# Optimization experiments

Measured on AMD Instinct MI355X. Metric: run time of the kernel, lower is better.

Reference implementation:

```python
import jax, jax.numpy as jnp
import numpy as np

S, IN, OUT = 2048, 512, 512
H, KV = 16, 4            # query heads, kv heads (cross-broadcast + averaged)
DQ = DK = DV = 64        # per-head embedding dims


def setup_inputs() -> dict:
    key = jax.random.key(0)
    ks = jax.random.split(key, 5)
    lim_in = 1.0 / np.sqrt(IN)
    lim_o = 1.0 / np.sqrt(H * DV)
    x = jax.random.normal(ks[0], (S, IN), dtype=jnp.float32)
    Wq = jax.random.uniform(ks[1], (H * DQ, IN), jnp.float32, -lim_in, lim_in)
    Wk = jax.random.uniform(ks[2], (KV * DK, IN), jnp.float32, -lim_in, lim_in)
    Wv = jax.random.uniform(ks[3], (KV * DV, IN), jnp.float32, -lim_in, lim_in)
    Wo = jax.random.uniform(ks[4], (OUT, H * DV), jnp.float32, -lim_o, lim_o)
    return {"x": x, "Wq": Wq, "Wk": Wk, "Wv": Wv, "Wo": Wo}


def reference(x, Wq, Wk, Wv, Wo):
    seq = x.shape[0]
    # projections (eqx.nn.Linear: y = W @ x, no bias)
    q = (x @ Wq.T).reshape(seq, H, DQ)    # [S, H, DQ]
    k = (x @ Wk.T).reshape(seq, KV, DK)   # [S, KV, DK]
    v = (x @ Wv.T).reshape(seq, KV, DV)   # [S, KV, DV]
    # cross-broadcast every kv head against every query head -> [KV, H, S, S]
    scores = jnp.einsum('shd,tkd->khst', q, k) / jnp.sqrt(jnp.asarray(DK, x.dtype))
    # NOTE: original applies causal mask whenever `mask is not None`; the
    # boolean flag is always passed, so masking is effectively always on.
    causal = jnp.tril(jnp.ones((seq, seq), dtype=bool))
    scores = jnp.where(causal, scores, -jnp.inf)
    w = jax.nn.softmax(scores, axis=-1)   # [KV, H, S, S]
    # attn @ V, then sum over kv heads and average by KV
    o = jnp.einsum('khst,tkd->shd', w, v) / KV  # [S, H, DV]
    return o.reshape(seq, H * DV) @ Wo.T        # [S, OUT]
```

## Files before the change

### kernel.cpp

```cpp
#include <hip/hip_runtime.h>
#include <hip/hip_bf16.h>

#define SEQ   2048
#define INF_  512
#define HQ    16
#define KVH   4
#define DH    64
#define NQ    (HQ*DH)
#define NKV   (KVH*DH)
#define OUTD  512

typedef short v8s __attribute__((ext_vector_type(8)));
typedef float v4f __attribute__((ext_vector_type(4)));

static __device__ __forceinline__ float bf2f(unsigned short u) {
    union { unsigned int i; float f; } c;
    c.i = ((unsigned int)u) << 16;
    return c.f;
}
static __device__ __forceinline__ unsigned short f2bf(float f) {
    union { float f; unsigned int i; } c; c.f = f;
    unsigned int lsb = (c.i >> 16) & 1u;
    c.i += 0x7fffu + lsb;
    return (unsigned short)(c.i >> 16);
}
static __device__ __forceinline__ unsigned int f2bf2(float lo, float hi) {
    union { __hip_bfloat162 h; unsigned int u; } c;
    c.h = __float22bfloat162_rn(make_float2(lo, hi));
    return c.u;
}
static __device__ __forceinline__ v8s pack8(v4f a, v4f b) {
    union { v8s s; uint4 u; } c;
    c.u = make_uint4(f2bf2(a[0], a[1]), f2bf2(a[2], a[3]),
                     f2bf2(b[0], b[1]), f2bf2(b[2], b[3]));
    return c.s;
}

static __device__ __forceinline__ void gll16(const void* g, void* l) {
    __builtin_amdgcn_global_load_lds(
        (const __attribute__((address_space(1))) void*)g,
        (__attribute__((address_space(3))) void*)l, 16, 0, 0);
}

static __device__ __forceinline__ void stage_tile(
    const unsigned short* __restrict__ src, int stride, int kb,
    unsigned short* ldsbase, int w, int lane)
{
#pragma unroll
    for (int i = 0; i < 2; i++) {
        const int rl = w * 16 + i * 8 + (lane >> 3);
        const int kc = ((lane & 7) ^ (rl & 7)) * 8;
        gll16(src + (size_t)rl * stride + kb + kc,
              ldsbase + (w * 16 + i * 8) * 64);
    }
}

#define QSCALE 0.180336880f

__global__ __launch_bounds__(256) void cast_all(
    const float* __restrict__ x,  const float* __restrict__ Wq,
    const float* __restrict__ Wk, const float* __restrict__ Wv,
    const float* __restrict__ Wo,
    unsigned short* __restrict__ xb,  unsigned short* __restrict__ Wqb,
    unsigned short* __restrict__ Wkb, unsigned short* __restrict__ Wvb,
    unsigned short* __restrict__ Wob)
{
    size_t i = ((size_t)blockIdx.x * 256 + threadIdx.x) * 8;
    const float* s; unsigned short* d; size_t off;
    if (i < 1048576)      { s = x;  d = xb;  off = i; }
    else if (i < 1572864) { s = Wq; d = Wqb; off = i - 1048576; }
    else if (i < 1703936) { s = Wk; d = Wkb; off = i - 1572864; }
    else if (i < 1835008) { s = Wv; d = Wvb; off = i - 1703936; }
    else                  { s = Wo; d = Wob; off = i - 1835008; }
    float4 a = *(const float4*)(s + off);
    float4 b = *(const float4*)(s + off + 4);
    *(uint4*)(d + off) = make_uint4(f2bf2(a.x, a.y), f2bf2(a.z, a.w),
                                    f2bf2(b.x, b.y), f2bf2(b.z, b.w));
}

__global__ __launch_bounds__(256, 4) void gemm_qkv(
    const unsigned short* __restrict__ xb,
    const unsigned short* __restrict__ Wqb,
    const unsigned short* __restrict__ Wkb,
    const unsigned short* __restrict__ Wvb,
    unsigned short* __restrict__ Qg,
    unsigned short* __restrict__ Kg,
    unsigned short* __restrict__ Vg)
{
    __shared__ unsigned short Asb[2][4096];
    __shared__ unsigned short Bsb[2][4096];

    const int m0 = blockIdx.x * 64;
    const int n0 = blockIdx.y * 64;

    const unsigned short* Bp; int role;
    if (n0 < NQ)            { Bp = Wqb + (size_t)n0 * INF_;              role = 0; }
    else if (n0 < NQ + NKV) { Bp = Wkb + (size_t)(n0 - NQ) * INF_;       role = 1; }
    else                    { Bp = Wvb + (size_t)(n0 - NQ - NKV) * INF_; role = 2; }

    const int tid = threadIdx.x;
    const int w = tid >> 6, lane = tid & 63;
    const int n = lane & 15, quad = lane >> 4;
    const int m7 = n & 7;
    const int r0w = (w & 1) * 32, c0w = (w >> 1) * 32;
    const unsigned short* Ap = xb + (size_t)m0 * INF_;

    v4f acc[2][2];
#pragma unroll
    for (int rt = 0; rt < 2; rt++)
#pragma unroll
        for (int ct = 0; ct < 2; ct++) acc[rt][ct] = (v4f){0.f,0.f,0.f,0.f};

    stage_tile(Ap, INF_, 0, &Asb[0][0], w, lane);
    stage_tile(Bp, INF_, 0, &Bsb[0][0], w, lane);

    for (int kb = 0; kb < INF_; kb += 64) {
        const int buf = (kb >> 6) & 1;
        __syncthreads();
        if (kb + 64 < INF_) {
            stage_tile(Ap, INF_, kb + 64, &Asb[buf ^ 1][0], w, lane);
            stage_tile(Bp, INF_, kb + 64, &Bsb[buf ^ 1][0], w, lane);
        }
#pragma unroll
        for (int kk = 0; kk < 2; kk++) {
            const int gs = ((kk * 4 + quad) ^ m7) * 8;
            v8s a0 = *(const v8s*)&Asb[buf][(r0w + n) * 64 + gs];
            v8s a1 = *(const v8s*)&Asb[buf][(r0w + 16 + n) * 64 + gs];
            v8s b0 = *(const v8s*)&Bsb[buf][(c0w + n) * 64 + gs];
            v8s b1 = *(const v8s*)&Bsb[buf][(c0w + 16 + n) * 64 + gs];
            acc[0][0] = __builtin_amdgcn_mfma_f32_16x16x32_bf16(a0, b0, acc[0][0], 0, 0, 0);
            acc[0][1] = __builtin_amdgcn_mfma_f32_16x16x32_bf16(a0, b1, acc[0][1], 0, 0, 0);
            acc[1][0] = __builtin_amdgcn_mfma_f32_16x16x32_bf16(a1, b0, acc[1][0], 0, 0, 0);
            acc[1][1] = __builtin_amdgcn_mfma_f32_16x16x32_bf16(a1, b1, acc[1][1], 0, 0, 0);
        }
    }

    const int t = m0 >> 6;
    if (role == 0) {
        unsigned short* base = Qg + ((size_t)(t * 16 + (n0 >> 6))) * 4096;
#pragma unroll
        for (int rt = 0; rt < 2; rt++)
#pragma unroll
            for (int ct = 0; ct < 2; ct++)
#pragma unroll
                for (int reg = 0; reg < 4; reg++) {
                    const int r = r0w + rt * 16 + quad * 4 + reg;
                    const int d = c0w + ct * 16 + n;
                    base[r * 64 + (((d >> 3) ^ (r & 7)) * 8) + (d & 7)] =
                        f2bf(acc[rt][ct][reg] * QSCALE);
                }
    } else if (role == 1) {
        const int g = (n0 - NQ) >> 6;
        unsigned short* base = Kg + ((size_t)(g * 32 + t)) * 4096;
#pragma unroll
        for (int rt = 0; rt < 2; rt++)
#pragma unroll
            for (int ct = 0; ct < 2; ct++)
#pragma unroll
                for (int reg = 0; reg < 4; reg++) {
                    const int r = r0w + rt * 16 + quad * 4 + reg;
                    const int d = c0w + ct * 16 + n;
                    base[r * 64 + (((d >> 3) ^ (r & 7)) * 8) + (d & 7)] =
                        f2bf(acc[rt][ct][reg]);
                }
    } else {
        const int g = (n0 - NQ - NKV) >> 6;
        unsigned short* base = Vg + ((size_t)(g * 32 + t)) * 4096;
#pragma unroll
        for (int rt = 0; rt < 2; rt++)
#pragma unroll
            for (int ct = 0; ct < 2; ct++) {
                const int jb_ = r0w + rt * 16 + quad * 4;
                const int d = c0w + ct * 16 + n;
                const int p = (jb_ & 32) + (((jb_ >> 2) & 3) * 8) + (((jb_ >> 4) & 1) * 4);
                *(uint2*)&base[d * 64 + (((p >> 3) ^ (d & 7)) * 8) + (p & 7)] =
                    make_uint2(f2bf2(acc[rt][ct][0], acc[rt][ct][1]),
                               f2bf2(acc[rt][ct][2], acc[rt][ct][3]));
            }
    }
}

__global__ __launch_bounds__(256, 4) void attn_mfma(
    const unsigned short* __restrict__ Qg,
    const unsigned short* __restrict__ Kg,
    const unsigned short* __restrict__ Vg,
    unsigned short* __restrict__ Oh)
{
    __shared__ unsigned short Ksb[2][4096];
    __shared__ unsigned short Vsb[2][4096];

    const int bx = blockIdx.x;
    const int h  = bx & 15;
    const int jj = (bx >> 4) & 15;
    const int g  = bx >> 8;
    const int jj2 = (jj + 8 * (g >> 1)) & 15;
    const int qi2 = (g & 1) ? (15 - jj2) : jj2;
    const int q0 = qi2 * 128;
    const int tid = threadIdx.x;
    const int w = tid >> 6, lane = tid & 63;
    const int n = lane & 15, quad = lane >> 4;
    const int r0 = w * 32;
    const int m7 = n & 7;
    const int ntile = 2 * qi2 + 2;

    {
        const size_t off = ((size_t)(g * 32)) * 4096 + w * 1024 + lane * 8;
        gll16(Kg + off,       &Ksb[0][w * 1024]);
        gll16(Kg + off + 512, &Ksb[0][w * 1024 + 512]);
        gll16(Vg + off,       &Vsb[0][w * 1024]);
        gll16(Vg + off + 512, &Vsb[0][w * 1024 + 512]);
    }

    v8s qf[2][2];
    {
        const unsigned short* tb =
            Qg + ((size_t)((2 * qi2 + (r0 >> 6)) * 16 + h)) * 4096 + (r0 & 63) * 64;
#pragma unroll
        for (int qt = 0; qt < 2; qt++) {
            const unsigned short* rp = tb + (qt * 16 + n) * 64;
            qf[qt][0] = *(const v8s*)(rp + (quad ^ m7) * 8);
            qf[qt][1] = *(const v8s*)(rp + ((quad + 4) ^ m7) * 8);
        }
    }

    v8s ones;
#pragma unroll
    for (int i = 0; i < 8; i++) ones[i] = (short)0x3F80;

    v4f Lacc[2];
    Lacc[0] = (v4f){0.f,0.f,0.f,0.f};
    Lacc[1] = (v4f){0.f,0.f,0.f,0.f};
    v4f Oacc[2][4];
#pragma unroll
    for (int qt = 0; qt < 2; qt++)
#pragma unroll
        for (int dt = 0; dt < 4; dt++) Oacc[qt][dt] = (v4f){0.f,0.f,0.f,0.f};
    const v4f z = (v4f){0.f,0.f,0.f,0.f};

    for (int tt = 0; tt < ntile; tt++) {
        const int buf = tt & 1;
        __syncthreads();
        if (tt + 1 < ntile) {
            const size_t off = ((size_t)(g * 32 + tt + 1)) * 4096 + w * 1024 + lane * 8;
            const int nb = buf ^ 1;
            gll16(Kg + off,       &Ksb[nb][w * 1024]);
            gll16(Kg + off + 512, &Ksb[nb][w * 1024 + 512]);
            gll16(Vg + off,       &Vsb[nb][w * 1024]);
            gll16(Vg + off + 512, &Vsb[nb][w * 1024 + 512]);
        }
        const int t0 = tt * 64;
        const bool do0 = (t0 <= q0 + r0 + 15);
        const bool do1 = (t0 <= q0 + r0 + 31);
        if (!do1) continue;

        const unsigned short* Kb = Ksb[buf];
        const unsigned short* Vb = Vsb[buf];

        v4f sc[2][4];
#pragma unroll
        for (int jt = 0; jt < 4; jt++) {
            const int kr = (jt * 16 + n) * 64;
            v8s kf0 = *(const v8s*)&Kb[kr + (quad ^ m7) * 8];
            v8s kf1 = *(const v8s*)&Kb[kr + ((quad + 4) ^ m7) * 8];
            if (do0) {
                v4f tq = __builtin_amdgcn_mfma_f32_16x16x32_bf16(kf0, qf[0][0], z, 0, 0, 0);
                sc[0][jt] = __builtin_amdgcn_mfma_f32_16x16x32_bf16(kf1, qf[0][1], tq, 0, 0, 0);
            }
            v4f t1 = __builtin_amdgcn_mfma_f32_16x16x32_bf16(kf0, qf[1][0], z, 0, 0, 0);
            sc[1][jt] = __builtin_amdgcn_mfma_f32_16x16x32_bf16(kf1, qf[1][1], t1, 0, 0, 0);
        }

#pragma unroll
        for (int qt = 0; qt < 2; qt++) {
            if (qt == 0 && !do0) continue;
            const int qg = q0 + r0 + qt * 16 + n;
            if (t0 + 63 > q0 + r0 + qt * 16) {
#pragma unroll
                for (int jt = 0; jt < 4; jt++) {
                    const int jg = t0 + jt * 16 + quad * 4;
#pragma unroll
                    for (int reg = 0; reg < 4; reg++)
                        sc[qt][jt][reg] = (jg + reg <= qg) ? sc[qt][jt][reg] : -INFINITY;
                }
            }
#pragma unroll
            for (int jt = 0; jt < 4; jt++)
#pragma unroll
                for (int reg = 0; reg < 4; reg++)
                    sc[qt][jt][reg] = __builtin_amdgcn_exp2f(sc[qt][jt][reg]);
        }

        v8s pf[2][2];
        if (do0) {
            pf[0][0] = pack8(sc[0][0], sc[0][1]);
            pf[0][1] = pack8(sc[0][2], sc[0][3]);
        }
        pf[1][0] = pack8(sc[1][0], sc[1][1]);
        pf[1][1] = pack8(sc[1][2], sc[1][3]);

        if (do0) {
            Lacc[0] = __builtin_amdgcn_mfma_f32_16x16x32_bf16(ones, pf[0][0], Lacc[0], 0, 0, 0);
            Lacc[0] = __builtin_amdgcn_mfma_f32_16x16x32_bf16(ones, pf[0][1], Lacc[0], 0, 0, 0);
        }
        Lacc[1] = __builtin_amdgcn_mfma_f32_16x16x32_bf16(ones, pf[1][0], Lacc[1], 0, 0, 0);
        Lacc[1] = __builtin_amdgcn_mfma_f32_16x16x32_bf16(ones, pf[1][1], Lacc[1], 0, 0, 0);

#pragma unroll
        for (int dt = 0; dt < 4; dt++) {
            const int vr = (dt * 16 + n) * 64;
            v8s vf0 = *(const v8s*)&Vb[vr + (quad ^ m7) * 8];
            v8s vf1 = *(const v8s*)&Vb[vr + ((quad + 4) ^ m7) * 8];
            if (do0) {
                Oacc[0][dt] = __builtin_amdgcn_mfma_f32_16x16x32_bf16(vf0, pf[0][0], Oacc[0][dt], 0, 0, 0);
                Oacc[0][dt] = __builtin_amdgcn_mfma_f32_16x16x32_bf16(vf1, pf[0][1], Oacc[0][dt], 0, 0, 0);
            }
            Oacc[1][dt] = __builtin_amdgcn_mfma_f32_16x16x32_bf16(vf0, pf[1][0], Oacc[1][dt], 0, 0, 0);
            Oacc[1][dt] = __builtin_amdgcn_mfma_f32_16x16x32_bf16(vf1, pf[1][1], Oacc[1][dt], 0, 0, 0);
        }
    }

    unsigned short* Ohp = Oh + (size_t)g * ((size_t)SEQ * NQ);
#pragma unroll
    for (int qt = 0; qt < 2; qt++) {
        const float inv = 0.25f / Lacc[qt][0];
        const int row = q0 + r0 + qt * 16 + n;
        unsigned short* dst = Ohp + (size_t)row * NQ + h * DH + quad * 4;
#pragma unroll
        for (int dt = 0; dt < 4; dt++) {
            uint2 pk = make_uint2(f2bf2(Oacc[qt][dt][0] * inv, Oacc[qt][dt][1] * inv),
                                  f2bf2(Oacc[qt][dt][2] * inv, Oacc[qt][dt][3] * inv));
            *(uint2*)(dst + dt * 16) = pk;
        }
    }
}

__global__ __launch_bounds__(256, 4) void gemm_out(
    const unsigned short* __restrict__ Oh,
    const unsigned short* __restrict__ Wob,
    float* __restrict__ C)
{
    __shared__ unsigned short Asb[32][72];
    __shared__ unsigned short Bsb[64][72];

    const int m0 = blockIdx.x * 32;
    const int n0 = blockIdx.y * 64;
    const int tid = threadIdx.x;
    const int w = tid >> 6, lane = tid & 63;
    const int n = lane & 15, quad = lane >> 4;
    const int rw = (w & 1) * 16, cw = (w >> 1) * 32;
    const int ar = tid >> 3, akc = (tid & 7) * 8;
    const int br = tid >> 2, bkc = (tid & 3) * 16;

    v4f acc[2];
    acc[0] = (v4f){0.f,0.f,0.f,0.f};
    acc[1] = (v4f){0.f,0.f,0.f,0.f};

    const size_t plane = (size_t)SEQ * NQ;
    const size_t abase = (size_t)(m0 + ar) * NQ + akc;
    const unsigned short* bp = Wob + (size_t)(n0 + br) * NQ + bkc;

    uint4 ua[4];
#pragma unroll
    for (int g = 0; g < 4; g++) ua[g] = *(const uint4*)(Oh + g * plane + abase);
    uint4 ub0 = *(const uint4*)(bp), ub1 = *(const uint4*)(bp + 8);

    for (int kb = 0; kb < NQ; kb += 64) {
        __syncthreads();
        {
            unsigned int ow[4];
#pragma unroll
            for (int q = 0; q < 4; q++) {
                const unsigned int u0 = ((const unsigned int*)&ua[0])[q];
                const unsigned int u1 = ((const unsigned int*)&ua[1])[q];
                const unsigned int u2 = ((const unsigned int*)&ua[2])[q];
                const unsigned int u3 = ((const unsigned int*)&ua[3])[q];
                float lo = bf2f((unsigned short)(u0 & 0xffffu)) + bf2f((unsigned short)(u1 & 0xffffu))
                         + bf2f((unsigned short)(u2 & 0xffffu)) + bf2f((unsigned short)(u3 & 0xffffu));
                float hi = bf2f((unsigned short)(u0 >> 16)) + bf2f((unsigned short)(u1 >> 16))
                         + bf2f((unsigned short)(u2 >> 16)) + bf2f((unsigned short)(u3 >> 16));
                ow[q] = f2bf2(lo, hi);
            }
            *(uint4*)&Asb[ar][akc] = make_uint4(ow[0], ow[1], ow[2], ow[3]);
        }
        *(uint4*)&Bsb[br][bkc]     = ub0;
        *(uint4*)&Bsb[br][bkc + 8] = ub1;
        __syncthreads();
        if (kb + 64 < NQ) {
#pragma unroll
            for (int g = 0; g < 4; g++)
                ua[g] = *(const uint4*)(Oh + g * plane + abase + kb + 64);
            ub0 = *(const uint4*)(bp + kb + 64);
            ub1 = *(const uint4*)(bp + kb + 64 + 8);
        }
#pragma unroll
        for (int kk = 0; kk < 2; kk++) {
            v8s a  = *(const v8s*)&Asb[rw + n][kk * 32 + quad * 8];
            v8s b0 = *(const v8s*)&Bsb[cw + n][kk * 32 + quad * 8];
            v8s b1 = *(const v8s*)&Bsb[cw + 16 + n][kk * 32 + quad * 8];
            acc[0] = __builtin_amdgcn_mfma_f32_16x16x32_bf16(a, b0, acc[0], 0, 0, 0);
            acc[1] = __builtin_amdgcn_mfma_f32_16x16x32_bf16(a, b1, acc[1], 0, 0, 0);
        }
    }

#pragma unroll
    for (int ct = 0; ct < 2; ct++)
#pragma unroll
        for (int reg = 0; reg < 4; reg++) {
            const int row = m0 + rw + quad * 4 + reg;
            const int col = n0 + cw + ct * 16 + n;
            C[(size_t)row * OUTD + col] = acc[ct][reg];
        }
}

extern "C" void kernel_launch(void* const* d_in, const int* in_sizes, int n_in,
                              void* d_out, int out_size, void* d_ws, size_t ws_size,
                              hipStream_t stream) {
    const float* x  = (const float*)d_in[0];
    const float* Wq = (const float*)d_in[1];
    const float* Wk = (const float*)d_in[2];
    const float* Wv = (const float*)d_in[3];
    const float* Wo = (const float*)d_in[4];
    float* out = (float*)d_out;

    char* base = (char*)d_ws;
    unsigned short* Oh  = (unsigned short*)(base);
    unsigned short* xb  = (unsigned short*)(base);
    unsigned short* Wqb = (unsigned short*)(base + 2097152);
    unsigned short* Wkb = (unsigned short*)(base + 3145728);
    unsigned short* Wvb = (unsigned short*)(base + 3407872);
    unsigned short* Qg  = (unsigned short*)(base + 16777216);
    unsigned short* Kg  = (unsigned short*)(base + 20971520);
    unsigned short* Vg  = (unsigned short*)(base + 22020096);
    unsigned short* Wob = (unsigned short*)(base + 23068672);

    dim3 blk(256);
    cast_all<<<dim3(1152), blk, 0, stream>>>(x, Wq, Wk, Wv, Wo,
                                             xb, Wqb, Wkb, Wvb, Wob);
    gemm_qkv<<<dim3(SEQ / 64, (NQ + 2 * NKV) / 64), blk, 0, stream>>>(
        xb, Wqb, Wkb, Wvb, Qg, Kg, Vg);
    attn_mfma<<<dim3(1024), blk, 0, stream>>>(Qg, Kg, Vg, Oh);
    gemm_out<<<dim3(SEQ / 32, OUTD / 64), blk, 0, stream>>>(Oh, Wob, out);
}
```

Measured before the change: 142.4 us.

## Split KV-head reduction into separate kernel and async-stage gemm_out tiles

The four per-KV-head partial outputs are now summed by a standalone sum4 kernel into a single bf16 buffer that reuses the Q workspace. gemm_out then stages A and B tiles through LDS with global_load_lds double buffering and an XOR swizzle, instead of register loads followed by a 4-way reduction. The attention kernel also hoists the V fragment loads ahead of the softmax and raises wave priority around the MFMA blocks. This adds a kernel launch and an extra write and read of the summed buffer, in exchange for a simpler, better-pipelined output GEMM that reads one plane instead of four.

```diff
diff --git a/kernel.cpp b/kernel.cpp
--- a/kernel.cpp
+++ b/kernel.cpp
@@ -53,6 +53,16 @@
         gll16(src + (size_t)rl * stride + kb + kc,
               ldsbase + (w * 16 + i * 8) * 64);
     }
+}
+
+static __device__ __forceinline__ void stage_tile32(
+    const unsigned short* __restrict__ src, int stride, int kb,
+    unsigned short* ldsbase, int w, int lane)
+{
+    const int rl = w * 8 + (lane >> 3);
+    const int kc = ((lane & 7) ^ (rl & 7)) * 8;
+    gll16(src + (size_t)rl * stride + kb + kc,
+          ldsbase + (w * 8) * 64);
 }
 
 #define QSCALE 0.180336880f
@@ -257,6 +267,7 @@
         const unsigned short* Vb = Vsb[buf];
 
         v4f sc[2][4];
+        __builtin_amdgcn_s_setprio(1);
 #pragma unroll
         for (int jt = 0; jt < 4; jt++) {
             const int kr = (jt * 16 + n) * 64;
@@ -269,6 +280,15 @@
             v4f t1 = __builtin_amdgcn_mfma_f32_16x16x32_bf16(kf0, qf[1][0], z, 0, 0, 0);
             sc[1][jt] = __builtin_amdgcn_mfma_f32_16x16x32_bf16(kf1, qf[1][1], t1, 0, 0, 0);
         }
+        __builtin_amdgcn_s_setprio(0);
+
+        v8s vf[4][2];
+#pragma unroll
+        for (int dt = 0; dt < 4; dt++) {
+            const int vr = (dt * 16 + n) * 64;
+            vf[dt][0] = *(const v8s*)&Vb[vr + (quad ^ m7) * 8];
+            vf[dt][1] = *(const v8s*)&Vb[vr + ((quad + 4) ^ m7) * 8];
+        }
 
 #pragma unroll
         for (int qt = 0; qt < 2; qt++) {
@@ -298,6 +318,7 @@
         pf[1][0] = pack8(sc[1][0], sc[1][1]);
         pf[1][1] = pack8(sc[1][2], sc[1][3]);
 
+        __builtin_amdgcn_s_setprio(1);
         if (do0) {
             Lacc[0] = __builtin_amdgcn_mfma_f32_16x16x32_bf16(ones, pf[0][0], Lacc[0], 0, 0, 0);
             Lacc[0] = __builtin_amdgcn_mfma_f32_16x16x32_bf16(ones, pf[0][1], Lacc[0], 0, 0, 0);
@@ -307,16 +328,14 @@
 
 #pragma unroll
         for (int dt = 0; dt < 4; dt++) {
-            const int vr = (dt * 16 + n) * 64;
-            v8s vf0 = *(const v8s*)&Vb[vr + (quad ^ m7) * 8];
-            v8s vf1 = *(const v8s*)&Vb[vr + ((quad + 4) ^ m7) * 8];
             if (do0) {
-                Oacc[0][dt] = __builtin_amdgcn_mfma_f32_16x16x32_bf16(vf0, pf[0][0], Oacc[0][dt], 0, 0, 0);
-                Oacc[0][dt] = __builtin_amdgcn_mfma_f32_16x16x32_bf16(vf1, pf[0][1], Oacc[0][dt], 0, 0, 0);
+                Oacc[0][dt] = __builtin_amdgcn_mfma_f32_16x16x32_bf16(vf[dt][0], pf[0][0], Oacc[0][dt], 0, 0, 0);
+                Oacc[0][dt] = __builtin_amdgcn_mfma_f32_16x16x32_bf16(vf[dt][1], pf[0][1], Oacc[0][dt], 0, 0, 0);
             }
-            Oacc[1][dt] = __builtin_amdgcn_mfma_f32_16x16x32_bf16(vf0, pf[1][0], Oacc[1][dt], 0, 0, 0);
-            Oacc[1][dt] = __builtin_amdgcn_mfma_f32_16x16x32_bf16(vf1, pf[1][1], Oacc[1][dt], 0, 0, 0);
-        }
+            Oacc[1][dt] = __builtin_amdgcn_mfma_f32_16x16x32_bf16(vf[dt][0], pf[1][0], Oacc[1][dt], 0, 0, 0);
+            Oacc[1][dt] = __builtin_amdgcn_mfma_f32_16x16x32_bf16(vf[dt][1], pf[1][1], Oacc[1][dt], 0, 0, 0);
+        }
+        __builtin_amdgcn_s_setprio(0);
     }
 
     unsigned short* Ohp = Oh + (size_t)g * ((size_t)SEQ * NQ);
@@ -334,69 +353,71 @@
     }
 }
 
+__global__ __launch_bounds__(256) void sum4(
+    const unsigned short* __restrict__ Oh,
+    unsigned short* __restrict__ Os)
+{
+    const size_t i = ((size_t)blockIdx.x * 256 + threadIdx.x) * 8;
+    const size_t plane = (size_t)SEQ * NQ;
+    uint4 u0 = *(const uint4*)(Oh + i);
+    uint4 u1 = *(const uint4*)(Oh + plane + i);
+    uint4 u2 = *(const uint4*)(Oh + 2 * plane + i);
+    uint4 u3 = *(const uint4*)(Oh + 3 * plane + i);
+    unsigned int ow[4];
+#pragma unroll
+    for (int q = 0; q < 4; q++) {
+        const unsigned int a = ((const unsigned int*)&u0)[q];
+        const unsigned int b = ((const unsigned int*)&u1)[q];
+        const unsigned int c = ((const unsigned int*)&u2)[q];
+        const unsigned int d = ((const unsigned int*)&u3)[q];
+        float lo = bf2f((unsigned short)(a & 0xffffu)) + bf2f((unsigned short)(b & 0xffffu))
+                 + bf2f((unsigned short)(c & 0xffffu)) + bf2f((unsigned short)(d & 0xffffu));
+        float hi = bf2f((unsigned short)(a >> 16)) + bf2f((unsigned short)(b >> 16))
+                 + bf2f((unsigned short)(c >> 16)) + bf2f((unsigned short)(d >> 16));
+        ow[q] = f2bf2(lo, hi);
+    }
+    *(uint4*)(Os + i) = make_uint4(ow[0], ow[1], ow[2], ow[3]);
+}
+
 __global__ __launch_bounds__(256, 4) void gemm_out(
-    const unsigned short* __restrict__ Oh,
+    const unsigned short* __restrict__ Os,
     const unsigned short* __restrict__ Wob,
     float* __restrict__ C)
 {
-    __shared__ unsigned short Asb[32][72];
-    __shared__ unsigned short Bsb[64][72];
+    __shared__ unsigned short Asb[2][2048];
+    __shared__ unsigned short Bsb[2][4096];
 
     const int m0 = blockIdx.x * 32;
     const int n0 = blockIdx.y * 64;
     const int tid = threadIdx.x;
     const int w = tid >> 6, lane = tid & 63;
     const int n = lane & 15, quad = lane >> 4;
+    const int m7 = n & 7;
     const int rw = (w & 1) * 16, cw = (w >> 1) * 32;
-    const int ar = tid >> 3, akc = (tid & 7) * 8;
-    const int br = tid >> 2, bkc = (tid & 3) * 16;
+
+    const unsigned short* Ap = Os + (size_t)m0 * NQ;
+    const unsigned short* Bp = Wob + (size_t)n0 * NQ;
 
     v4f acc[2];
     acc[0] = (v4f){0.f,0.f,0.f,0.f};
     acc[1] = (v4f){0.f,0.f,0.f,0.f};
 
-    const size_t plane = (size_t)SEQ * NQ;
-    const size_t abase = (size_t)(m0 + ar) * NQ + akc;
-    const unsigned short* bp = Wob + (size_t)(n0 + br) * NQ + bkc;
-
-    uint4 ua[4];
-#pragma unroll
-    for (int g = 0; g < 4; g++) ua[g] = *(const uint4*)(Oh + g * plane + abase);
-    uint4 ub0 = *(const uint4*)(bp), ub1 = *(const uint4*)(bp + 8);
+    stage_tile32(Ap, NQ, 0, &Asb[0][0], w, lane);
+    stage_tile  (Bp, NQ, 0, &Bsb[0][0], w, lane);
 
     for (int kb = 0; kb < NQ; kb += 64) {
-        __syncthreads();
-        {
-            unsigned int ow[4];
-#pragma unroll
-            for (int q = 0; q < 4; q++) {
-                const unsigned int u0 = ((const unsigned int*)&ua[0])[q];
-                const unsigned int u1 = ((const unsigned int*)&ua[1])[q];
-                const unsigned int u2 = ((const unsigned int*)&ua[2])[q];
-                const unsigned int u3 = ((const unsigned int*)&ua[3])[q];
-                float lo = bf2f((unsigned short)(u0 & 0xffffu)) + bf2f((unsigned short)(u1 & 0xffffu))
-                         + bf2f((unsigned short)(u2 & 0xffffu)) + bf2f((unsigned short)(u3 & 0xffffu));
-                float hi = bf2f((unsigned short)(u0 >> 16)) + bf2f((unsigned short)(u1 >> 16))
-                         + bf2f((unsigned short)(u2 >> 16)) + bf2f((unsigned short)(u3 >> 16));
-                ow[q] = f2bf2(lo, hi);
-            }
-            *(uint4*)&Asb[ar][akc] = make_uint4(ow[0], ow[1], ow[2], ow[3]);
-        }
-        *(uint4*)&Bsb[br][bkc]     = ub0;
-        *(uint4*)&Bsb[br][bkc + 8] = ub1;
+        const int buf = (kb >> 6) & 1;
         __syncthreads();
         if (kb + 64 < NQ) {
-#pragma unroll
-            for (int g = 0; g < 4; g++)
-                ua[g] = *(const uint4*)(Oh + g * plane + abase + kb + 64);
-            ub0 = *(const uint4*)(bp + kb + 64);
-            ub1 = *(const uint4*)(bp + kb + 64 + 8);
+            stage_tile32(Ap, NQ, kb + 64, &Asb[buf ^ 1][0], w, lane);
+            stage_tile  (Bp, NQ, kb + 64, &Bsb[buf ^ 1][0], w, lane);
         }
 #pragma unroll
         for (int kk = 0; kk < 2; kk++) {
-            v8s a  = *(const v8s*)&Asb[rw + n][kk * 32 + quad * 8];
-            v8s b0 = *(const v8s*)&Bsb[cw + n][kk * 32 + quad * 8];
-            v8s b1 = *(const v8s*)&Bsb[cw + 16 + n][kk * 32 + quad * 8];
+            const int gs = ((kk * 4 + quad) ^ m7) * 8;
+            v8s a  = *(const v8s*)&Asb[buf][(rw + n) * 64 + gs];
+            v8s b0 = *(const v8s*)&Bsb[buf][(cw + n) * 64 + gs];
+            v8s b1 = *(const v8s*)&Bsb[buf][(cw + 16 + n) * 64 + gs];
             acc[0] = __builtin_amdgcn_mfma_f32_16x16x32_bf16(a, b0, acc[0], 0, 0, 0);
             acc[1] = __builtin_amdgcn_mfma_f32_16x16x32_bf16(a, b1, acc[1], 0, 0, 0);
         }
@@ -432,6 +453,7 @@
     unsigned short* Kg  = (unsigned short*)(base + 20971520);
     unsigned short* Vg  = (unsigned short*)(base + 22020096);
     unsigned short* Wob = (unsigned short*)(base + 23068672);
+    unsigned short* Os  = Qg;
 
     dim3 blk(256);
     cast_all<<<dim3(1152), blk, 0, stream>>>(x, Wq, Wk, Wv, Wo,
@@ -439,5 +461,6 @@
     gemm_qkv<<<dim3(SEQ / 64, (NQ + 2 * NKV) / 64), blk, 0, stream>>>(
         xb, Wqb, Wkb, Wvb, Qg, Kg, Vg);
     attn_mfma<<<dim3(1024), blk, 0, stream>>>(Qg, Kg, Vg, Oh);
-    gemm_out<<<dim3(SEQ / 32, OUTD / 64), blk, 0, stream>>>(Oh, Wob, out);
-}
+    sum4<<<dim3(1024), blk, 0, stream>>>(Oh, Os);
+    gemm_out<<<dim3(SEQ / 32, OUTD / 64), blk, 0, stream>>>(Os, Wob, out);
+}
```

Result: slower. 221.0 us (+55.2%).
